# Kernel optimization log

Measured on AMD Instinct MI355X. Metric: run time of the kernel, lower is better.

The kernel has to match this reference:

```python
import jax, jax.numpy as jnp
import numpy as np

EPS = 1e-5

def _ln(x, g, b):
    m = jnp.mean(x, axis=-1, keepdims=True)
    v = jnp.var(x, axis=-1, keepdims=True)
    return (x - m) / jnp.sqrt(v + EPS) * g + b

def setup_inputs() -> dict:
    key = jax.random.key(0)
    ks = jax.random.split(key, 16)
    B, N, CZ, C = 1, 512, 128, 16
    s_cz = 1.0 / np.sqrt(CZ)
    s_c = 1.0 / np.sqrt(C)
    def lin(k, fan_in, shape):
        return jax.random.uniform(k, shape, jnp.float32, -1.0, 1.0) / np.sqrt(fan_in)
    return {
        'x': jax.random.normal(ks[0], (B, N, N, CZ), jnp.float32),
        'Wa1': lin(ks[1], CZ, (CZ, C)), 'ba1': lin(ks[2], CZ, (C,)),
        'Wa2': lin(ks[3], CZ, (CZ, C)), 'ba2': lin(ks[4], CZ, (C,)),
        'Wb1': lin(ks[5], CZ, (CZ, C)), 'bb1': lin(ks[6], CZ, (C,)),
        'Wb2': lin(ks[7], CZ, (CZ, C)), 'bb2': lin(ks[8], CZ, (C,)),
        'ln2_g': jnp.ones((C,), jnp.float32), 'ln2_b': jnp.zeros((C,), jnp.float32),
        'Wg': lin(ks[9], CZ, (CZ, CZ)), 'bg': lin(ks[10], CZ, (CZ,)),
        'Wz': lin(ks[11], C, (C, CZ)), 'bz': lin(ks[12], C, (CZ,)),
    }

def reference(x, Wa1, ba1, Wa2, ba2, Wb1, bb1, Wb2, bb2, ln2_g, ln2_b, Wg, bg, Wz, bz):
    # NOTE: original code computes z=ln1(x) then overwrites z=x, so ln1 is a no-op.
    direction = 'outgoing'
    a = jax.nn.sigmoid((x @ Wa1 + ba1) * (x @ Wa2 + ba2))  # [B,N,N,c]
    b = jax.nn.sigmoid((x @ Wb1 + bb1) * (x @ Wb2 + bb2))  # [B,N,N,c]
    if direction == 'incoming':
        a = jnp.swapaxes(a, 1, 2)
        b = jnp.swapaxes(b, 1, 2)
    g = jax.nn.sigmoid(x @ Wg + bg)  # [B,N,N,c_z]
    # z[b,i,j,c] = sum_k a[b,i,k,c] * b[b,k,j,c]  (per-channel triangle matmul)
    z = jnp.einsum('bikc,bkjc->bijc', a, b)
    return g * (_ln(z, ln2_g, ln2_b) @ Wz + bz)
```

## Files before the change

### kernel.cpp

```cpp
#include <hip/hip_runtime.h>


#define NN 512
#define PP (NN*NN)
#define CZD 128
#define CD 16
#define LN_EPS 1e-5f

typedef unsigned short u16;
typedef __bf16 bf16x8 __attribute__((ext_vector_type(8)));
typedef float  f32x4  __attribute__((ext_vector_type(4)));

#define OFF_A  0u
#define OFF_B  8388608u
#define OFF_Z  16777216u
#define OFF_G  33554432u
#define OFF_WT 100663296u
#define OFF_BC 100712448u

__device__ __forceinline__ float bf2f(u16 u) {
    union { unsigned int i; float f; } v; v.i = ((unsigned int)u) << 16; return v.f;
}
__device__ __forceinline__ u16 f2bf(float f) {
    union { float f; unsigned int i; } v; v.f = f;
    unsigned int r = (v.i + 0x7FFFu + ((v.i >> 16) & 1u)) >> 16;
    return (u16)r;
}
__device__ __forceinline__ float sigmoidf(float x) { return 1.0f / (1.0f + __expf(-x)); }

__device__ __forceinline__ int swz(int row, int bytecol) {
    return row * 256 + (bytecol ^ ((row & 7) << 4));
}

__global__ void pack_w(const float* __restrict__ Wa1, const float* __restrict__ Wa2,
                       const float* __restrict__ Wb1, const float* __restrict__ Wb2,
                       const float* __restrict__ Wg,
                       const float* __restrict__ ba1, const float* __restrict__ ba2,
                       const float* __restrict__ bb1, const float* __restrict__ bb2,
                       const float* __restrict__ bg,
                       u16* __restrict__ wt, float* __restrict__ bc) {
    int idx = blockIdx.x * 256 + threadIdx.x;
    int n = idx >> 7, k = idx & 127;
    float v;
    if      (n < 16) v = Wa1[k * CD + n];
    else if (n < 32) v = Wa2[k * CD + (n - 16)];
    else if (n < 48) v = Wb1[k * CD + (n - 32)];
    else if (n < 64) v = Wb2[k * CD + (n - 48)];
    else             v = Wg [k * CZD + (n - 64)];
    wt[n * CZD + k] = f2bf(v);
    if (idx < 192) {
        float b;
        if      (idx < 16) b = ba1[idx];
        else if (idx < 32) b = ba2[idx - 16];
        else if (idx < 48) b = bb1[idx - 32];
        else if (idx < 64) b = bb2[idx - 48];
        else               b = bg [idx - 64];
        bc[idx] = b;
    }
}

__global__ __launch_bounds__(512, 4) void proj_kernel(const float* __restrict__ x,
                                                      const u16* __restrict__ wt,
                                                      const float* __restrict__ bc,
                                                      u16* __restrict__ a_ws, u16* __restrict__ b_ws,
                                                      u16* __restrict__ g_ws) {
    extern __shared__ __align__(16) char lds[];
    char* Wl = lds;
    char* Xl = lds + 49152;
    char* aT = lds;
    char* bT = lds + 4096;
    char* gT = lds + 49152;
    const int t = threadIdx.x;
    const int wv = t >> 6, lane = t & 63, l16 = lane & 15, quad = lane >> 4;
    const long pos0 = (long)blockIdx.x * 128;

#pragma unroll
    for (int i = 0; i < 6; ++i) {
        int c = t + 512 * i;
        int n = c >> 4, g = c & 15;
        uint4 v = *reinterpret_cast<const uint4*>(wt + n * CZD + g * 8);
        *reinterpret_cast<uint4*>(Wl + swz(n, g * 16)) = v;
    }
#pragma unroll
    for (int i = 0; i < 8; ++i) {
        int c = t + 512 * i;
        int r = c >> 5, c4 = c & 31;
        const float4 v = *reinterpret_cast<const float4*>(x + (pos0 + r) * CZD + c4 * 4);
        u16 tmp[4] = { f2bf(v.x), f2bf(v.y), f2bf(v.z), f2bf(v.w) };
        *reinterpret_cast<uint2*>(Xl + swz(r, c4 * 8)) = *reinterpret_cast<const uint2*>(tmp);
    }
    __syncthreads();

    f32x4 acc[12];
#pragma unroll
    for (int ct = 0; ct < 12; ++ct) acc[ct] = (f32x4){0.f, 0.f, 0.f, 0.f};
    bf16x8 af[4];
#pragma unroll
    for (int ks = 0; ks < 4; ++ks)
        af[ks] = *reinterpret_cast<const bf16x8*>(Xl + swz(wv * 16 + l16, ks * 64 + quad * 16));
#pragma unroll
    for (int ks = 0; ks < 4; ++ks)
#pragma unroll
        for (int ct = 0; ct < 12; ++ct) {
            bf16x8 wb = *reinterpret_cast<const bf16x8*>(Wl + swz(ct * 16 + l16, ks * 64 + quad * 16));
            acc[ct] = __builtin_amdgcn_mfma_f32_16x16x32_bf16(af[ks], wb, acc[ct], 0, 0, 0);
        }
    __syncthreads();

    {
        const float ba1 = bc[l16], ba2 = bc[16 + l16], bb1 = bc[32 + l16], bb2 = bc[48 + l16];
        u16 av[4], bv[4];
#pragma unroll
        for (int r = 0; r < 4; ++r) {
            av[r] = f2bf(sigmoidf((acc[0][r] + ba1) * (acc[1][r] + ba2)));
            bv[r] = f2bf(sigmoidf((acc[2][r] + bb1) * (acc[3][r] + bb2)));
        }
        *reinterpret_cast<uint2*>(aT + swz(l16, wv * 32 + quad * 8)) = *reinterpret_cast<const uint2*>(av);
        *reinterpret_cast<uint2*>(bT + swz(l16, wv * 32 + quad * 8)) = *reinterpret_cast<const uint2*>(bv);
#pragma unroll
        for (int ct = 0; ct < 8; ++ct) {
            const float bgv = bc[64 + ct * 16 + l16];
#pragma unroll
            for (int r = 0; r < 4; ++r) {
                int pos = wv * 16 + quad * 4 + r;
                *reinterpret_cast<u16*>(gT + swz(pos, ct * 32 + l16 * 2)) =
                    f2bf(sigmoidf(acc[4 + ct][r] + bgv));
            }
        }
    }
    __syncthreads();

    if (t < 256) {
        int ch = t >> 4, i = t & 15;
        uint4 v = *reinterpret_cast<const uint4*>(aT + swz(ch, i * 16));
        *reinterpret_cast<uint4*>(a_ws + (long)ch * PP + pos0 + i * 8) = v;
    } else {
        int u = t - 256;
        int ch = u >> 4, i = u & 15;
        uint4 v = *reinterpret_cast<const uint4*>(bT + swz(ch, i * 16));
        *reinterpret_cast<uint4*>(b_ws + (long)ch * PP + pos0 + i * 8) = v;
    }
#pragma unroll
    for (int i = 0; i < 4; ++i) {
        int c = t + 512 * i;
        int pos = c >> 4, g = c & 15;
        uint4 v = *reinterpret_cast<const uint4*>(gT + swz(pos, g * 16));
        *reinterpret_cast<uint4*>(g_ws + (pos0 + pos) * CZD + g * 8) = v;
    }
}

__global__ __launch_bounds__(256) void tri_kernel(const u16* __restrict__ a_ws,
                                                  const u16* __restrict__ b_ws,
                                                  float* __restrict__ z_ws) {
    __shared__ __align__(16) u16 Alds[64][72];
    __shared__ __align__(16) u16 Btl[64][72];
    const int t = threadIdx.x;
    const int wave = t >> 6, lane = t & 63, l16 = lane & 15, quad = lane >> 4;
    const int c = blockIdx.y;
    const int i0 = (blockIdx.x >> 3) * 64, j0 = (blockIdx.x & 7) * 64;
    const u16* Ap = a_ws + (long)c * PP;
    const u16* Bp = b_ws + (long)c * PP;

    f32x4 acc[4];
#pragma unroll
    for (int ct = 0; ct < 4; ++ct) acc[ct] = (f32x4){0.f, 0.f, 0.f, 0.f};

    for (int k0 = 0; k0 < NN; k0 += 64) {
#pragma unroll
        for (int i = 0; i < 2; ++i) {
            int chunk = t + 256 * i;
            int r = chunk >> 3, ko = (chunk & 7) << 3;
            uint4 v = *reinterpret_cast<const uint4*>(Ap + (long)(i0 + r) * NN + k0 + ko);
            *reinterpret_cast<uint4*>(&Alds[r][ko]) = v;
        }
#pragma unroll
        for (int i = 0; i < 2; ++i) {
            int chunk = t + 256 * i;
            int j = chunk & 63, kg = chunk >> 6;
            u16 tmp[8];
#pragma unroll
            for (int kk = 0; kk < 8; ++kk)
                tmp[kk] = Bp[(long)(k0 + kg * 8 + kk) * NN + j0 + j];
            *reinterpret_cast<uint4*>(&Btl[j][(kg ^ (j & 7)) << 3]) = *reinterpret_cast<uint4*>(tmp);
        }
        __syncthreads();
#pragma unroll
        for (int kk = 0; kk < 64; kk += 32) {
            bf16x8 af = *reinterpret_cast<const bf16x8*>(&Alds[wave * 16 + l16][kk + quad * 8]);
            int kc = (kk >> 3) + quad;
#pragma unroll
            for (int ct = 0; ct < 4; ++ct) {
                int n = ct * 16 + l16;
                bf16x8 bfv = *reinterpret_cast<const bf16x8*>(&Btl[n][(kc ^ (n & 7)) << 3]);
                acc[ct] = __builtin_amdgcn_mfma_f32_16x16x32_bf16(af, bfv, acc[ct], 0, 0, 0);
            }
        }
        __syncthreads();
    }
    float* Zp = z_ws + (long)c * PP;
#pragma unroll
    for (int ct = 0; ct < 4; ++ct)
#pragma unroll
        for (int r = 0; r < 4; ++r)
            Zp[(long)(i0 + wave * 16 + quad * 4 + r) * NN + j0 + ct * 16 + l16] = acc[ct][r];
}

__global__ __launch_bounds__(256) void out_kernel(const float* __restrict__ z_ws,
                                                  const u16* __restrict__ g_ws,
                                                  const float* __restrict__ Wz, const float* __restrict__ bz,
                                                  const float* __restrict__ lng, const float* __restrict__ lnb,
                                                  float* __restrict__ out) {
    __shared__ __align__(16) float zt[16][72];
    __shared__ __align__(16) float nl[64][20];
    __shared__ __align__(16) float wz[16][128];
    __shared__ float bzl[128];
    __shared__ float lg[16], lb[16];
    const int t = threadIdx.x;
    const long pos0 = (long)blockIdx.x * 64;

    {
        int cc = t >> 4, off = (t & 15) << 2;
        const float4 v = *reinterpret_cast<const float4*>(z_ws + (long)cc * PP + pos0 + off);
        *reinterpret_cast<float4*>(&zt[cc][off]) = v;
    }
#pragma unroll
    for (int i = 0; i < 8; ++i) {
        int idx = t + 256 * i;
        wz[idx >> 7][idx & 127] = Wz[idx];
    }
    if (t < 128)      bzl[t] = bz[t];
    else if (t < 144) lg[t - 128] = lng[t - 128];
    else if (t < 160) lb[t - 144] = lnb[t - 144];
    __syncthreads();

    {
        int p = t & 63, cgr = t >> 6;
        float m = 0.f;
#pragma unroll
        for (int c0 = 0; c0 < 16; ++c0) m += zt[c0][p];
        m *= (1.f / 16.f);
        float v = 0.f;
#pragma unroll
        for (int c0 = 0; c0 < 16; ++c0) { float d = zt[c0][p] - m; v += d * d; }
        v *= (1.f / 16.f);
        float s = rsqrtf(v + LN_EPS);
#pragma unroll
        for (int cc = 0; cc < 4; ++cc) {
            int c0 = cgr * 4 + cc;
            nl[p][c0] = (zt[c0][p] - m) * s * lg[c0] + lb[c0];
        }
    }
    __syncthreads();

    const int cz = t & 127, pg = t >> 7;
    float wzr[16];
#pragma unroll
    for (int c0 = 0; c0 < 16; ++c0) wzr[c0] = wz[c0][cz];
    const float bzv = bzl[cz];
#pragma unroll
    for (int pp2 = 0; pp2 < 32; ++pp2) {
        int p = pg * 32 + pp2;
        const float4* np = reinterpret_cast<const float4*>(&nl[p][0]);
        float y = bzv;
#pragma unroll
        for (int c4 = 0; c4 < 4; ++c4) {
            float4 nv = np[c4];
            y += nv.x * wzr[c4 * 4 + 0] + nv.y * wzr[c4 * 4 + 1] +
                 nv.z * wzr[c4 * 4 + 2] + nv.w * wzr[c4 * 4 + 3];
        }
        long o = (pos0 + p) * CZD + cz;
        float gv = bf2f(g_ws[o]);
        out[o] = gv * y;
    }
}

extern "C" void kernel_launch(void* const* d_in, const int* in_sizes, int n_in,
                              void* d_out, int out_size, void* d_ws, size_t ws_size,
                              hipStream_t stream) {
    const float* x   = (const float*)d_in[0];
    const float* Wa1 = (const float*)d_in[1];
    const float* ba1 = (const float*)d_in[2];
    const float* Wa2 = (const float*)d_in[3];
    const float* ba2 = (const float*)d_in[4];
    const float* Wb1 = (const float*)d_in[5];
    const float* bb1 = (const float*)d_in[6];
    const float* Wb2 = (const float*)d_in[7];
    const float* bb2 = (const float*)d_in[8];
    const float* lng = (const float*)d_in[9];
    const float* lnb = (const float*)d_in[10];
    const float* Wg  = (const float*)d_in[11];
    const float* bg  = (const float*)d_in[12];
    const float* Wz  = (const float*)d_in[13];
    const float* bz  = (const float*)d_in[14];
    float* out = (float*)d_out;
    char* ws = (char*)d_ws;
    u16*   a_ws = (u16*)(ws + OFF_A);
    u16*   b_ws = (u16*)(ws + OFF_B);
    float* z_ws = (float*)(ws + OFF_Z);
    u16*   g_ws = (u16*)(ws + OFF_G);
    u16*   wt   = (u16*)(ws + OFF_WT);
    float* bc   = (float*)(ws + OFF_BC);

    hipLaunchKernelGGL(pack_w, dim3(96), dim3(256), 0, stream,
                       Wa1, Wa2, Wb1, Wb2, Wg, ba1, ba2, bb1, bb2, bg, wt, bc);
    hipLaunchKernelGGL(proj_kernel, dim3(2048), dim3(512), 81920, stream, x, wt, bc, a_ws, b_ws, g_ws);
    hipLaunchKernelGGL(tri_kernel, dim3(64, 16), dim3(256), 0, stream, a_ws, b_ws, z_ws);
    hipLaunchKernelGGL(out_kernel, dim3(4096), dim3(256), 0, stream, z_ws, g_ws, Wz, bz, lng, lnb, out);
}
```

Before: 321.9 us.

## Enlarge triangle matmul tiles to 128x128 with coalesced B staging; widen output kernel

The triangle kernel now uses 512-thread blocks computing 128x128 tiles, with each wave holding a 4x2 grid of MFMA accumulators so A and B fragments are reused across more multiplies. B is loaded with coalesced 16-byte row reads into LDS and then transposed inside LDS, replacing the scalar strided global gathers. A gets an XOR swizzle in LDS. The output kernel processes 128 positions per 512-thread block, with each thread writing two channels as float2 and reading paired bf16 gate values. The trade-offs are an extra LDS pass and barrier per k-step and fewer blocks (256) for the triangle stage.

```diff
diff --git a/kernel.cpp b/kernel.cpp
--- a/kernel.cpp
+++ b/kernel.cpp
@@ -149,84 +149,107 @@
     }
 }
 
-__global__ __launch_bounds__(256) void tri_kernel(const u16* __restrict__ a_ws,
+__global__ __launch_bounds__(512) void tri_kernel(const u16* __restrict__ a_ws,
                                                   const u16* __restrict__ b_ws,
                                                   float* __restrict__ z_ws) {
-    __shared__ __align__(16) u16 Alds[64][72];
-    __shared__ __align__(16) u16 Btl[64][72];
+    __shared__ __align__(16) char Alds[16384];
+    __shared__ __align__(16) char Btl [16384];
+    __shared__ __align__(16) char Brow[16384];
     const int t = threadIdx.x;
-    const int wave = t >> 6, lane = t & 63, l16 = lane & 15, quad = lane >> 4;
+    const int wv = t >> 6, lane = t & 63, l16 = lane & 15, quad = lane >> 4;
+    const int wr = wv >> 2, wc = wv & 3;
     const int c = blockIdx.y;
-    const int i0 = (blockIdx.x >> 3) * 64, j0 = (blockIdx.x & 7) * 64;
+    const int i0 = (blockIdx.x >> 2) * 128, j0 = (blockIdx.x & 3) * 128;
     const u16* Ap = a_ws + (long)c * PP;
     const u16* Bp = b_ws + (long)c * PP;
 
-    f32x4 acc[4];
-#pragma unroll
-    for (int ct = 0; ct < 4; ++ct) acc[ct] = (f32x4){0.f, 0.f, 0.f, 0.f};
+    f32x4 acc[4][2];
+#pragma unroll
+    for (int m = 0; m < 4; ++m)
+#pragma unroll
+        for (int n = 0; n < 2; ++n) acc[m][n] = (f32x4){0.f, 0.f, 0.f, 0.f};
 
     for (int k0 = 0; k0 < NN; k0 += 64) {
 #pragma unroll
         for (int i = 0; i < 2; ++i) {
-            int chunk = t + 256 * i;
-            int r = chunk >> 3, ko = (chunk & 7) << 3;
+            int ch = t + 512 * i;
+            int r = ch >> 3, ko = (ch & 7) * 8;
             uint4 v = *reinterpret_cast<const uint4*>(Ap + (long)(i0 + r) * NN + k0 + ko);
-            *reinterpret_cast<uint4*>(&Alds[r][ko]) = v;
+            *reinterpret_cast<uint4*>(Alds + r * 128 + ((ko * 2) ^ ((r & 7) << 4))) = v;
         }
 #pragma unroll
         for (int i = 0; i < 2; ++i) {
-            int chunk = t + 256 * i;
-            int j = chunk & 63, kg = chunk >> 6;
-            u16 tmp[8];
-#pragma unroll
-            for (int kk = 0; kk < 8; ++kk)
-                tmp[kk] = Bp[(long)(k0 + kg * 8 + kk) * NN + j0 + j];
-            *reinterpret_cast<uint4*>(&Btl[j][(kg ^ (j & 7)) << 3]) = *reinterpret_cast<uint4*>(tmp);
+            int ch = t + 512 * i;
+            int k = ch >> 4, jo = (ch & 15) * 8;
+            uint4 v = *reinterpret_cast<const uint4*>(Bp + (long)(k0 + k) * NN + j0 + jo);
+            *reinterpret_cast<uint4*>(Brow + k * 256 + jo * 2) = v;
         }
         __syncthreads();
 #pragma unroll
-        for (int kk = 0; kk < 64; kk += 32) {
-            bf16x8 af = *reinterpret_cast<const bf16x8*>(&Alds[wave * 16 + l16][kk + quad * 8]);
-            int kc = (kk >> 3) + quad;
-#pragma unroll
-            for (int ct = 0; ct < 4; ++ct) {
-                int n = ct * 16 + l16;
-                bf16x8 bfv = *reinterpret_cast<const bf16x8*>(&Btl[n][(kc ^ (n & 7)) << 3]);
-                acc[ct] = __builtin_amdgcn_mfma_f32_16x16x32_bf16(af, bfv, acc[ct], 0, 0, 0);
+        for (int i = 0; i < 2; ++i) {
+            int ch = t + 512 * i;
+            int j = ch & 127, kg = ch >> 7;
+            union { u16 s[8]; uint4 v; } tb;
+#pragma unroll
+            for (int m = 0; m < 8; ++m)
+                tb.s[m] = *reinterpret_cast<const u16*>(Brow + (kg * 8 + m) * 256 + j * 2);
+            *reinterpret_cast<uint4*>(Btl + j * 128 + ((kg ^ (j & 7)) << 4)) = tb.v;
+        }
+        __syncthreads();
+#pragma unroll
+        for (int ks = 0; ks < 2; ++ks) {
+            bf16x8 af[4];
+#pragma unroll
+            for (int m = 0; m < 4; ++m) {
+                int row = wr * 64 + m * 16 + l16;
+                af[m] = *reinterpret_cast<const bf16x8*>(
+                    Alds + row * 128 + ((ks * 64 + quad * 16) ^ ((row & 7) << 4)));
             }
+#pragma unroll
+            for (int n = 0; n < 2; ++n) {
+                int jrow = wc * 32 + n * 16 + l16;
+                bf16x8 bf = *reinterpret_cast<const bf16x8*>(
+                    Btl + jrow * 128 + (((ks * 4 + quad) ^ (jrow & 7)) << 4));
+#pragma unroll
+                for (int m = 0; m < 4; ++m)
+                    acc[m][n] = __builtin_amdgcn_mfma_f32_16x16x32_bf16(af[m], bf, acc[m][n], 0, 0, 0);
+            }
         }
         __syncthreads();
     }
     float* Zp = z_ws + (long)c * PP;
 #pragma unroll
-    for (int ct = 0; ct < 4; ++ct)
-#pragma unroll
-        for (int r = 0; r < 4; ++r)
-            Zp[(long)(i0 + wave * 16 + quad * 4 + r) * NN + j0 + ct * 16 + l16] = acc[ct][r];
-}
-
-__global__ __launch_bounds__(256) void out_kernel(const float* __restrict__ z_ws,
+    for (int m = 0; m < 4; ++m)
+#pragma unroll
+        for (int n = 0; n < 2; ++n)
+#pragma unroll
+            for (int r = 0; r < 4; ++r)
+                Zp[(long)(i0 + wr * 64 + m * 16 + quad * 4 + r) * NN + j0 + wc * 32 + n * 16 + l16]
+                    = acc[m][n][r];
+}
+
+__global__ __launch_bounds__(512) void out_kernel(const float* __restrict__ z_ws,
                                                   const u16* __restrict__ g_ws,
                                                   const float* __restrict__ Wz, const float* __restrict__ bz,
                                                   const float* __restrict__ lng, const float* __restrict__ lnb,
                                                   float* __restrict__ out) {
-    __shared__ __align__(16) float zt[16][72];
-    __shared__ __align__(16) float nl[64][20];
-    __shared__ __align__(16) float wz[16][128];
+    __shared__ __align__(16) float zt[16][128];
+    __shared__ __align__(16) float nl[128][20];
+    __shared__ __align__(16) float wzs[16][128];
     __shared__ float bzl[128];
     __shared__ float lg[16], lb[16];
     const int t = threadIdx.x;
-    const long pos0 = (long)blockIdx.x * 64;
+    const long pos0 = (long)blockIdx.x * 128;
 
     {
-        int cc = t >> 4, off = (t & 15) << 2;
-        const float4 v = *reinterpret_cast<const float4*>(z_ws + (long)cc * PP + pos0 + off);
-        *reinterpret_cast<float4*>(&zt[cc][off]) = v;
-    }
-#pragma unroll
-    for (int i = 0; i < 8; ++i) {
-        int idx = t + 256 * i;
-        wz[idx >> 7][idx & 127] = Wz[idx];
+        int ch = t >> 5, off = (t & 31) * 4;
+        const float4 v = *reinterpret_cast<const float4*>(z_ws + (long)ch * PP + pos0 + off);
+        *reinterpret_cast<float4*>(&zt[ch][off]) = v;
+    }
+    {
+        int idx = t * 4;
+        const float4 v = *reinterpret_cast<const float4*>(Wz + idx);
+        *reinterpret_cast<float4*>(&wzs[idx >> 7][idx & 127]) = v;
     }
     if (t < 128)      bzl[t] = bz[t];
     else if (t < 144) lg[t - 128] = lng[t - 128];
@@ -234,7 +257,7 @@
     __syncthreads();
 
     {
-        int p = t & 63, cgr = t >> 6;
+        int p = t & 127, cgr = t >> 7;
         float m = 0.f;
 #pragma unroll
         for (int c0 = 0; c0 < 16; ++c0) m += zt[c0][p];
@@ -252,25 +275,34 @@
     }
     __syncthreads();
 
-    const int cz = t & 127, pg = t >> 7;
-    float wzr[16];
-#pragma unroll
-    for (int c0 = 0; c0 < 16; ++c0) wzr[c0] = wz[c0][cz];
-    const float bzv = bzl[cz];
-#pragma unroll
-    for (int pp2 = 0; pp2 < 32; ++pp2) {
-        int p = pg * 32 + pp2;
+    const int czp = (t & 63) * 2, pg = t >> 6;
+    float wzr[32];
+#pragma unroll
+    for (int c0 = 0; c0 < 16; ++c0) {
+        wzr[2 * c0]     = wzs[c0][czp];
+        wzr[2 * c0 + 1] = wzs[c0][czp + 1];
+    }
+    const float bz0 = bzl[czp], bz1 = bzl[czp + 1];
+    const unsigned int* gp = reinterpret_cast<const unsigned int*>(g_ws);
+#pragma unroll
+    for (int pp2 = 0; pp2 < 16; ++pp2) {
+        int p = pg * 16 + pp2;
         const float4* np = reinterpret_cast<const float4*>(&nl[p][0]);
-        float y = bzv;
+        float y0 = bz0, y1 = bz1;
 #pragma unroll
         for (int c4 = 0; c4 < 4; ++c4) {
             float4 nv = np[c4];
-            y += nv.x * wzr[c4 * 4 + 0] + nv.y * wzr[c4 * 4 + 1] +
-                 nv.z * wzr[c4 * 4 + 2] + nv.w * wzr[c4 * 4 + 3];
-        }
-        long o = (pos0 + p) * CZD + cz;
-        float gv = bf2f(g_ws[o]);
-        out[o] = gv * y;
+            y0 += nv.x * wzr[(c4 * 4 + 0) * 2] + nv.y * wzr[(c4 * 4 + 1) * 2] +
+                  nv.z * wzr[(c4 * 4 + 2) * 2] + nv.w * wzr[(c4 * 4 + 3) * 2];
+            y1 += nv.x * wzr[(c4 * 4 + 0) * 2 + 1] + nv.y * wzr[(c4 * 4 + 1) * 2 + 1] +
+                  nv.z * wzr[(c4 * 4 + 2) * 2 + 1] + nv.w * wzr[(c4 * 4 + 3) * 2 + 1];
+        }
+        long o = (pos0 + p) * CZD + czp;
+        unsigned int gg = gp[o >> 1];
+        float g0 = bf2f((u16)(gg & 0xffffu));
+        float g1 = bf2f((u16)(gg >> 16));
+        float2 res; res.x = g0 * y0; res.y = g1 * y1;
+        *reinterpret_cast<float2*>(out + o) = res;
     }
 }
 
@@ -304,6 +336,6 @@
     hipLaunchKernelGGL(pack_w, dim3(96), dim3(256), 0, stream,
                        Wa1, Wa2, Wb1, Wb2, Wg, ba1, ba2, bb1, bb2, bg, wt, bc);
     hipLaunchKernelGGL(proj_kernel, dim3(2048), dim3(512), 81920, stream, x, wt, bc, a_ws, b_ws, g_ws);
-    hipLaunchKernelGGL(tri_kernel, dim3(64, 16), dim3(256), 0, stream, a_ws, b_ws, z_ws);
-    hipLaunchKernelGGL(out_kernel, dim3(4096), dim3(256), 0, stream, z_ws, g_ws, Wz, bz, lng, lnb, out);
-}
+    hipLaunchKernelGGL(tri_kernel, dim3(16, 16), dim3(512), 0, stream, a_ws, b_ws, z_ws);
+    hipLaunchKernelGGL(out_kernel, dim3(2048), dim3(512), 0, stream, z_ws, g_ws, Wz, bz, lng, lnb, out);
+}
```

Measured after the change: 321.9 us. Within noise of the previous version (+0.0%).
